# Optimization experiments

Hardware: AMD Instinct MI355X
Metric: run time of the kernel (lower is better)

Reference implementation:

```python
import jax, jax.numpy as jnp
import numpy as np

N, E, DIM, HID, LAYERS = 100000, 600000, 128, 256, 2
LN_EPS = 1e-5


def setup_inputs() -> dict:
    key = jax.random.key(0)
    ks = jax.random.split(key, 16)
    h = jax.random.normal(ks[0], (N, DIM), dtype=jnp.float32)
    edge_index = jax.random.randint(ks[1], (E, 2), 0, N, dtype=jnp.int64)
    edge_attr = jax.random.uniform(ks[2], (E, 1), dtype=jnp.float32)
    s = 0.02
    # edge MLP: Linear(2*DIM+1, HID) -> GELU -> Linear(HID, 1) -> Sigmoid
    edge_w1 = jax.random.normal(ks[3], (LAYERS, 2 * DIM + 1, HID), dtype=jnp.float32) * s
    edge_b1 = jnp.zeros((LAYERS, HID), dtype=jnp.float32)
    edge_w2 = jax.random.normal(ks[4], (LAYERS, HID, 1), dtype=jnp.float32) * s
    edge_b2 = jnp.zeros((LAYERS, 1), dtype=jnp.float32)
    # node MLP: Linear(2*DIM, HID) -> GELU -> Linear(HID, DIM)
    node_w1 = jax.random.normal(ks[5], (LAYERS, 2 * DIM, HID), dtype=jnp.float32) * s
    node_b1 = jnp.zeros((LAYERS, HID), dtype=jnp.float32)
    node_w2 = jax.random.normal(ks[6], (LAYERS, HID, DIM), dtype=jnp.float32) * s
    node_b2 = jnp.zeros((LAYERS, DIM), dtype=jnp.float32)
    ln_g = jnp.ones((LAYERS, DIM), dtype=jnp.float32)
    ln_b = jnp.zeros((LAYERS, DIM), dtype=jnp.float32)
    return {"h": h, "edge_index": edge_index, "edge_attr": edge_attr,
            "edge_w1": edge_w1, "edge_b1": edge_b1, "edge_w2": edge_w2, "edge_b2": edge_b2,
            "node_w1": node_w1, "node_b1": node_b1, "node_w2": node_w2, "node_b2": node_b2,
            "ln_g": ln_g, "ln_b": ln_b}


def _layernorm(x, g, b):
    mu = jnp.mean(x, axis=-1, keepdims=True)
    var = jnp.mean(jnp.square(x - mu), axis=-1, keepdims=True)
    return (x - mu) * jax.lax.rsqrt(var + LN_EPS) * g + b


def reference(h, edge_index, edge_attr, edge_w1, edge_b1, edge_w2, edge_b2,
              node_w1, node_b1, node_w2, node_b2, ln_g, ln_b):
    src = edge_index[:, 0]
    dst = edge_index[:, 1]
    n = h.shape[0]
    for i in range(LAYERS):
        h_src = h[src]                                  # [E, DIM]
        h_dst = h[dst]                                  # [E, DIM]
        x = jnp.concatenate([h_src, h_dst, edge_attr], axis=-1)  # [E, 2*DIM+1]
        g1 = jax.nn.gelu(x @ edge_w1[i] + edge_b1[i], approximate=False)
        gate = jax.nn.sigmoid(g1 @ edge_w2[i] + edge_b2[i])       # [E, 1]
        msg = h_src * gate                              # [E, DIM]
        agg = jax.ops.segment_sum(msg, dst, num_segments=n)       # [N, DIM]
        den = jax.ops.segment_sum(gate, dst, num_segments=n)      # [N, 1]
        agg = agg / jnp.maximum(den, 1e-6)
        u = jnp.concatenate([h, agg], axis=-1)          # [N, 2*DIM]
        upd = jax.nn.gelu(u @ node_w1[i] + node_b1[i], approximate=False) @ node_w2[i] + node_b2[i]
        h = _layernorm(h + upd, ln_g[i], ln_b[i])
    return h
```

## Files before the change

### kernel.cpp

```cpp
#include <hip/hip_runtime.h>
#include <math.h>

#define NNODE 100000
#define NEDGE 600000
#define DIM 128
#define HID 256
#define NLAYERS 2
#define PROJ_BLOCKS 1563

typedef short bf16x8 __attribute__((ext_vector_type(8)));
typedef short bf16x4 __attribute__((ext_vector_type(4)));
typedef float f32x4 __attribute__((ext_vector_type(4)));
typedef float f32x2 __attribute__((ext_vector_type(2)));

#define WK 136
#define WLD 264
#define LUTN 2048

__device__ __forceinline__ short f2bf(float x) {
    union { float f; unsigned u; } v; v.f = x;
    unsigned r = v.u + 0x7FFFu + ((v.u >> 16) & 1u);
    return (short)(r >> 16);
}
__device__ __forceinline__ float bf2f(short s) {
    union { unsigned u; float f; } v; v.u = ((unsigned)(unsigned short)s) << 16;
    return v.f;
}
__device__ __forceinline__ float gelu_fast(float x) {
    float e = exp2f(-2.4554673f * x);
    return x * __builtin_amdgcn_rcpf(1.0f + e);
}
__device__ __forceinline__ float lut_look(const float* __restrict__ lut, float x) {
    float t = fmaf(x, 128.f, 1024.5f);
    t = fminf(fmaxf(t, 0.f), 2047.f);
    return lut[(int)t];
}

__global__ void prep_weights(const float* __restrict__ ew1,
                             const float* __restrict__ eb1,
                             const float* __restrict__ ew2,
                             const float* __restrict__ nw1,
                             const float* __restrict__ nw2,
                             const float* __restrict__ h0,
                             const int* __restrict__ ei,
                             short* __restrict__ pW,
                             short* __restrict__ nW1T,
                             short* __restrict__ nW2T,
                             float* __restrict__ w1a_p,
                             float* __restrict__ b1_p,
                             float* __restrict__ w2_p,
                             short* __restrict__ hb,
                             unsigned char* __restrict__ h8,
                             float* __restrict__ luts,
                             int* __restrict__ deg)
{
    int idx = blockIdx.x * 256 + threadIdx.x;
    const int SZ1 = NLAYERS * 512 * 128;
    const int SZ2 = NLAYERS * 256 * 256;
    const int SZ3 = NLAYERS * 128 * 256;
    const int SZ4 = NLAYERS * 256;
    const int SZH = NNODE * DIM / 8;
    if (idx < SZ1) {
        int L = idx / (512 * 128); int rr = idx - L * 512 * 128;
        int r = rr >> 7, k = rr & 127;
        int srow = (r < 256) ? k : 128 + k;
        int scol = (r < 256) ? r : r - 256;
        pW[(size_t)L * 512 * WK + r * WK + k] = f2bf(ew1[(size_t)L * 257 * 256 + srow * 256 + scol]);
        return;
    }
    idx -= SZ1;
    if (idx < SZ2) {
        int L = idx >> 16, r = idx & 65535, n = r >> 8, k = r & 255;
        nW1T[(size_t)L * 256 * WLD + n * WLD + k] = f2bf(nw1[(size_t)L * 256 * 256 + k * 256 + n]);
        return;
    }
    idx -= SZ2;
    if (idx < SZ3) {
        int L = idx >> 15, r = idx & 32767, n = r >> 8, k = r & 255;
        nW2T[(size_t)L * 128 * WLD + n * WLD + k] = f2bf(nw2[(size_t)L * 256 * 128 + k * 128 + n]);
        return;
    }
    idx -= SZ3;
    if (idx < SZ4) {
        int L = idx >> 8, c = idx & 255;
        int cs = (c & ~63) | ((c & 3) * 16 + ((c >> 2) & 15));
        w1a_p[idx] = ew1[(size_t)L * 257 * 256 + 256 * 256 + cs];
        b1_p[idx]  = eb1[(size_t)L * 256 + cs];
        w2_p[idx]  = ew2[(size_t)L * 256 + cs];
        return;
    }
    idx -= SZ4;
    if (idx < SZH) {
        const float4* p = (const float4*)(h0 + (size_t)idx * 8);
        float4 a = p[0], b = p[1];
        bf16x8 t;
        t[0] = f2bf(a.x); t[1] = f2bf(a.y); t[2] = f2bf(a.z); t[3] = f2bf(a.w);
        t[4] = f2bf(b.x); t[5] = f2bf(b.y); t[6] = f2bf(b.z); t[7] = f2bf(b.w);
        *(bf16x8*)(hb + (size_t)idx * 8) = t;
        int wa = __builtin_amdgcn_cvt_pk_fp8_f32(a.x, a.y, 0, false);
        wa = __builtin_amdgcn_cvt_pk_fp8_f32(a.z, a.w, wa, true);
        int wb = __builtin_amdgcn_cvt_pk_fp8_f32(b.x, b.y, 0, false);
        wb = __builtin_amdgcn_cvt_pk_fp8_f32(b.z, b.w, wb, true);
        *(unsigned*)(h8 + (size_t)idx * 8) = (unsigned)wa;
        *(unsigned*)(h8 + (size_t)idx * 8 + 4) = (unsigned)wb;
        return;
    }
    idx -= SZH;
    if (idx < 2 * LUTN) {
        int i = idx & (LUTN - 1);
        float x = (float)(i - 1024) * (1.0f / 128.0f);
        float v;
        if (idx < LUTN) {
            v = 0.5f * x * (1.0f + erff(x * 0.70710678118654752f));
        } else {
            v = 1.0f / (1.0f + expf(-x));
        }
        luts[idx] = v;
        return;
    }
    idx -= 2 * LUTN;
    if (idx < NEDGE) {
        atomicAdd(&deg[ei[2 * idx + 1]], 1);
    }
}

__global__ void csr_scatter(const int* __restrict__ ei, const float* __restrict__ attr,
                            int* __restrict__ cursor, int2* __restrict__ epk) {
    int e = blockIdx.x * 256 + threadIdx.x;
    if (e >= NEDGE) return;
    int s = ei[2 * e], d = ei[2 * e + 1];
    int pos = atomicAdd(&cursor[d], 1);
    int2 pk; pk.x = s; pk.y = __float_as_int(attr[e]);
    epk[pos] = pk;
    if (e == 0) { int2 z; z.x = 0; z.y = 0; epk[NEDGE] = z; }
}

__device__ void scan_block512(const int* __restrict__ deg, int* __restrict__ rowptr,
                              int* __restrict__ cursor) {
    __shared__ int wsum[8];
    __shared__ int carry_s;
    const int tid = threadIdx.x, lane = tid & 63, wv = tid >> 6;
    if (tid == 0) carry_s = 0;
    __syncthreads();
    for (int base = 0; base < NNODE; base += 2048) {
        int i0 = base + tid * 4;
        int v0 = 0, v1 = 0, v2 = 0, v3 = 0;
        if (i0 + 3 < NNODE) {
            int4 q = *(const int4*)(deg + i0);
            v0 = q.x; v1 = q.y; v2 = q.z; v3 = q.w;
        } else if (i0 < NNODE) {
            v0 = deg[i0];
            if (i0 + 1 < NNODE) v1 = deg[i0 + 1];
            if (i0 + 2 < NNODE) v2 = deg[i0 + 2];
        }
        int tsum = v0 + v1 + v2 + v3;
        int x = tsum;
#pragma unroll
        for (int off = 1; off < 64; off <<= 1) {
            int y = __shfl_up(x, off);
            if (lane >= off) x += y;
        }
        if (lane == 63) wsum[wv] = x;
        __syncthreads();
        if (wv == 0) {
            int s = (lane < 8) ? wsum[lane] : 0;
#pragma unroll
            for (int off = 1; off < 8; off <<= 1) {
                int y = __shfl_up(s, off);
                if (lane >= off) s += y;
            }
            if (lane < 8) wsum[lane] = s;
        }
        __syncthreads();
        int carry = carry_s;
        int woff = wv ? wsum[wv - 1] : 0;
        int e0 = carry + woff + (x - tsum);
        if (i0 < NNODE)     { rowptr[i0] = e0;                cursor[i0] = e0; }
        if (i0 + 1 < NNODE) { int v = e0 + v0;                rowptr[i0+1] = v; cursor[i0+1] = v; }
        if (i0 + 2 < NNODE) { int v = e0 + v0 + v1;           rowptr[i0+2] = v; cursor[i0+2] = v; }
        if (i0 + 3 < NNODE) { int v = e0 + v0 + v1 + v2;      rowptr[i0+3] = v; cursor[i0+3] = v; }
        int total = wsum[7];
        __syncthreads();
        if (tid == 0) carry_s = carry + total;
        __syncthreads();
    }
    if (tid == 0) rowptr[NNODE] = carry_s;
}

__global__ __launch_bounds__(512, 2)
void proj_kernel(const short* __restrict__ hb,
                 const short* __restrict__ pW,
                 unsigned char* __restrict__ Ps8,
                 short* __restrict__ Pd,
                 const int* __restrict__ deg, int* __restrict__ rowptr,
                 int* __restrict__ cursor)
{
    if (blockIdx.x >= PROJ_BLOCKS) {
        scan_block512(deg, rowptr, cursor);
        return;
    }

    __shared__ short A[64][WK];
    const int tid = threadIdx.x;
    const int n0 = blockIdx.x * 64;

    for (int idx = tid; idx < 64 * 16; idx += 512) {
        int nl = idx >> 4, q = idx & 15;
        int gn = min(n0 + nl, NNODE - 1);
        *(bf16x8*)&A[nl][q * 8] = *(const bf16x8*)(hb + (size_t)gn * DIM + q * 8);
    }
    __syncthreads();

    const int lane = tid & 63;
    const int wv = tid >> 6;
    const int lrow = lane & 15;
    const int lkg = lane >> 4;

    f32x4 acc[4][4];
#pragma unroll
    for (int mi = 0; mi < 4; ++mi)
#pragma unroll
        for (int ni = 0; ni < 4; ++ni) acc[mi][ni] = (f32x4){0.f, 0.f, 0.f, 0.f};

    const short* xbase = &A[lrow][lkg * 8];
    const short* wbase = pW + (size_t)(wv * 64 + lrow) * WK + lkg * 8;

#pragma unroll
    for (int kt = 0; kt < 4; ++kt) {
        bf16x8 a[4], b[4];
#pragma unroll
        for (int mi = 0; mi < 4; ++mi)
            a[mi] = *(const bf16x8*)(xbase + mi * 16 * WK + kt * 32);
#pragma unroll
        for (int ni = 0; ni < 4; ++ni)
            b[ni] = *(const bf16x8*)(wbase + ni * 16 * WK + kt * 32);
#pragma unroll
        for (int mi = 0; mi < 4; ++mi)
#pragma unroll
            for (int ni = 0; ni < 4; ++ni)
                acc[mi][ni] = __builtin_amdgcn_mfma_f32_16x16x32_bf16(a[mi], b[ni], acc[mi][ni], 0, 0, 0);
    }

    const int cb = (wv & 3) * 64;
    if (wv < 4) {
#pragma unroll
        for (int mi = 0; mi < 4; ++mi)
#pragma unroll
            for (int reg = 0; reg < 4; ++reg) {
                int node = n0 + mi * 16 + lkg * 4 + reg;
                int w = __builtin_amdgcn_cvt_pk_fp8_f32(acc[mi][0][reg], acc[mi][1][reg], 0, false);
                w = __builtin_amdgcn_cvt_pk_fp8_f32(acc[mi][2][reg], acc[mi][3][reg], w, true);
                if (node < NNODE)
                    *(unsigned*)(Ps8 + (size_t)node * 256 + cb + lrow * 4) = (unsigned)w;
            }
    } else {
#pragma unroll
        for (int mi = 0; mi < 4; ++mi)
#pragma unroll
            for (int reg = 0; reg < 4; ++reg) {
                int node = n0 + mi * 16 + lkg * 4 + reg;
                bf16x4 t;
                t[0] = f2bf(acc[mi][0][reg]);
                t[1] = f2bf(acc[mi][1][reg]);
                t[2] = f2bf(acc[mi][2][reg]);
                t[3] = f2bf(acc[mi][3][reg]);
                if (node < NNODE)
                    *(bf16x4*)(Pd + (size_t)node * 256 + cb + lrow * 4) = t;
            }
    }
}

__global__ __launch_bounds__(256)
void edge_agg(const unsigned char* __restrict__ Ps8, const short* __restrict__ Pd,
              const unsigned char* __restrict__ h8,
              const int2* __restrict__ epk, const int* __restrict__ rowptr,
              const float* __restrict__ w1a_p, const float* __restrict__ b1_p,
              const float* __restrict__ w2_p, const float* __restrict__ b2,
              const float* __restrict__ luts,
              short* __restrict__ u2)
{
    __shared__ float sg[LUTN];
    __shared__ float ss[LUTN];

    const int tid = threadIdx.x;
#pragma unroll
    for (int i = 0; i < LUTN / 256; ++i) {
        sg[tid + i * 256] = luts[tid + i * 256];
        ss[tid + i * 256] = luts[LUTN + tid + i * 256];
    }
    __syncthreads();

    const int node = (blockIdx.x * 256 + tid) >> 6;
    const int lane = tid & 63;

    const int beg = __builtin_amdgcn_readfirstlane(rowptr[node]);
    const int end = __builtin_amdgcn_readfirstlane(rowptr[node + 1]);
    const int d = end - beg;

    const float4 w1av = ((const float4*)w1a_p)[lane];
    const float4 b1v  = ((const float4*)b1_p)[lane];
    const float4 w2v  = ((const float4*)w2_p)[lane];
    const float b2s = b2[0];

    bf16x4 pd = *(const bf16x4*)(Pd + (size_t)node * 256 + lane * 4);
    const float pb0 = bf2f(pd[0]) + b1v.x;
    const float pb1 = bf2f(pd[1]) + b1v.y;
    const float pb2 = bf2f(pd[2]) + b1v.z;
    const float pb3 = bf2f(pd[3]) + b1v.w;

    const unsigned pso = (unsigned)(lane * 4);
    const unsigned hvo = (unsigned)(lane * 2);

    float ax = 0.f, ay = 0.f, den = 0.f;

    if (d > 0) {
        const int dm = min(d, 64);
        const int dm1 = dm - 1;

        int2 sa0 = epk[beg + min(lane, d - 1)];
        int sl = sa0.x;
        float al = __int_as_float(sa0.y);

        auto gather = [&](int T, unsigned& PS, unsigned& HV) {
            int s_ = __shfl(sl, min(T, dm1));
            PS = *(const unsigned*)(Ps8 + (((unsigned)s_ << 8) + pso));
            HV = (unsigned)*(const unsigned short*)(h8 + (((unsigned)s_ << 7) + hvo));
        };
        auto edge_one = [&](float a, unsigned PSU, unsigned HVU) {
            f32x2 plo = __builtin_amdgcn_cvt_pk_f32_fp8((int)PSU, false);
            f32x2 phi = __builtin_amdgcn_cvt_pk_f32_fp8((int)PSU, true);
            float x0 = plo[0] + pb0 + a * w1av.x;
            float x1 = plo[1] + pb1 + a * w1av.y;
            float x2 = phi[0] + pb2 + a * w1av.z;
            float x3 = phi[1] + pb3 + a * w1av.w;
            float p = lut_look(sg, x0) * w2v.x + lut_look(sg, x1) * w2v.y +
                      lut_look(sg, x2) * w2v.z + lut_look(sg, x3) * w2v.w;
            p += __shfl_xor(p, 1);
            p += __shfl_xor(p, 2);
            p += __shfl_xor(p, 4);
            p += __shfl_xor(p, 8);
            p += __shfl_xor(p, 16);
            p += __shfl_xor(p, 32);
            float g = lut_look(ss, p + b2s);
            f32x2 hxy = __builtin_amdgcn_cvt_pk_f32_fp8((int)HVU, false);
            ax = fmaf(g, hxy[0], ax);
            ay = fmaf(g, hxy[1], ay);
            den += g;
        };

        unsigned pA0, pA1, pA2, pA3, hA0, hA1, hA2, hA3;
        unsigned pB0, pB1, pB2, pB3, hB0, hB1, hB2, hB3;
        gather(0, pA0, hA0); gather(1, pA1, hA1);
        gather(2, pA2, hA2); gather(3, pA3, hA3);

        for (int t = 0; t < dm; t += 4) {
            gather(t + 4, pB0, hB0); gather(t + 5, pB1, hB1);
            gather(t + 6, pB2, hB2); gather(t + 7, pB3, hB3);

            edge_one(__shfl(al, t), pA0, hA0);
            if (t + 1 < dm) edge_one(__shfl(al, t + 1), pA1, hA1);
            if (t + 2 < dm) edge_one(__shfl(al, t + 2), pA2, hA2);
            if (t + 3 < dm) edge_one(__shfl(al, t + 3), pA3, hA3);

            pA0 = pB0; pA1 = pB1; pA2 = pB2; pA3 = pB3;
            hA0 = hB0; hA1 = hB1; hA2 = hB2; hA3 = hB3;
        }

        for (int t2 = 64; t2 < d; ++t2) {
            int2 sa = epk[beg + t2];
            int s_ = __builtin_amdgcn_readfirstlane(sa.x);
            float a = __int_as_float(__builtin_amdgcn_readfirstlane(sa.y));
            unsigned PS = *(const unsigned*)(Ps8 + (((unsigned)s_ << 8) + pso));
            unsigned HV = (unsigned)*(const unsigned short*)(h8 + (((unsigned)s_ << 7) + hvo));
            edge_one(a, PS, HV);
        }
    }

    float dd = fmaxf(den, 1e-6f);
    float dinv = __builtin_amdgcn_rcpf(dd);
    dinv = dinv * (2.0f - dd * dinv);
    unsigned pk = (((unsigned)(unsigned short)f2bf(ay * dinv)) << 16) |
                  (unsigned)(unsigned short)f2bf(ax * dinv);
    *(unsigned*)(u2 + (size_t)node * 256 + lane * 2) = pk;
}

__global__ __launch_bounds__(256, 4)
void node_mlp(const float* __restrict__ hin,
              const short* __restrict__ hb,
              const short* __restrict__ u2,
              const short* __restrict__ W1T,
              const float* __restrict__ b1,
              const short* __restrict__ W2T,
              const float* __restrict__ b2,
              const float* __restrict__ lng, const float* __restrict__ lnb,
              float* __restrict__ hout, short* __restrict__ hb_out,
              unsigned char* __restrict__ h8_out)
{
    __shared__ short U[64][WLD];

    const int tid = threadIdx.x;
    const int n0 = blockIdx.x * 64;
    const int lane = tid & 63;
    const int wv = tid >> 6;

    for (int idx = tid; idx < 64 * 32; idx += 256) {
        int nl = idx >> 5, q = idx & 31;
        int gn = min(n0 + nl, NNODE - 1);
        const short* src = (q < 16) ? (hb + (size_t)gn * DIM + q * 8)
                                    : (u2 + (size_t)gn * 256 + (q - 16) * 8);
        *(bf16x8*)&U[nl][q * 8] = *(const bf16x8*)src;
    }
    __syncthreads();

    const int lrow = lane & 15;
    const int lkg = lane >> 4;
    const int n0w = wv * 64;

    f32x4 acc1[4][4];
#pragma unroll
    for (int mi = 0; mi < 4; ++mi)
#pragma unroll
        for (int ni = 0; ni < 4; ++ni) acc1[mi][ni] = (f32x4){0.f, 0.f, 0.f, 0.f};
    {
        const short* xbase = &U[lrow][lkg * 8];
        const short* wbase = W1T + (size_t)(n0w + lrow) * WLD + lkg * 8;
#pragma unroll
        for (int kt = 0; kt < 8; ++kt) {
            bf16x8 a[4], b[4];
#pragma unroll
            for (int mi = 0; mi < 4; ++mi)
                a[mi] = *(const bf16x8*)(xbase + mi * 16 * WLD + kt * 32);
#pragma unroll
            for (int ni = 0; ni < 4; ++ni)
                b[ni] = *(const bf16x8*)(wbase + ni * 16 * WLD + kt * 32);
#pragma unroll
            for (int mi = 0; mi < 4; ++mi)
#pragma unroll
                for (int ni = 0; ni < 4; ++ni)
                    acc1[mi][ni] = __builtin_amdgcn_mfma_f32_16x16x32_bf16(a[mi], b[ni], acc1[mi][ni], 0, 0, 0);
        }
    }
    __syncthreads();

    {
        float b1v[4];
#pragma unroll
        for (int ni = 0; ni < 4; ++ni) b1v[ni] = b1[n0w + ni * 16 + lrow];
#pragma unroll
        for (int mi = 0; mi < 4; ++mi)
#pragma unroll
            for (int ni = 0; ni < 4; ++ni)
#pragma unroll
                for (int reg = 0; reg < 4; ++reg) {
                    int row = mi * 16 + lkg * 4 + reg;
                    int col = n0w + ni * 16 + lrow;
                    U[row][col] = f2bf(gelu_fast(acc1[mi][ni][reg] + b1v[ni]));
                }
    }
    __syncthreads();

    f32x4 acc2[4][2];
#pragma unroll
    for (int mi = 0; mi < 4; ++mi)
#pragma unroll
        for (int ni = 0; ni < 2; ++ni) acc2[mi][ni] = (f32x4){0.f, 0.f, 0.f, 0.f};
    {
        const short* xbase = &U[lrow][lkg * 8];
        const short* wbase = W2T + (size_t)(wv * 32 + lrow) * WLD + lkg * 8;
#pragma unroll
        for (int kt = 0; kt < 8; ++kt) {
            bf16x8 a[4], b[2];
#pragma unroll
            for (int mi = 0; mi < 4; ++mi)
                a[mi] = *(const bf16x8*)(xbase + mi * 16 * WLD + kt * 32);
#pragma unroll
            for (int ni = 0; ni < 2; ++ni)
                b[ni] = *(const bf16x8*)(wbase + ni * 16 * WLD + kt * 32);
#pragma unroll
            for (int mi = 0; mi < 4; ++mi)
#pragma unroll
                for (int ni = 0; ni < 2; ++ni)
                    acc2[mi][ni] = __builtin_amdgcn_mfma_f32_16x16x32_bf16(a[mi], b[ni], acc2[mi][ni], 0, 0, 0);
        }
    }
    __syncthreads();

    float* R = (float*)&U[0][0];
    {
        float b2v[2];
#pragma unroll
        for (int ni = 0; ni < 2; ++ni) b2v[ni] = b2[wv * 32 + ni * 16 + lrow];
#pragma unroll
        for (int mi = 0; mi < 4; ++mi)
#pragma unroll
            for (int ni = 0; ni < 2; ++ni)
#pragma unroll
                for (int reg = 0; reg < 4; ++reg) {
                    int row = mi * 16 + lkg * 4 + reg;
                    int col = wv * 32 + ni * 16 + lrow;
                    R[row * 132 + col] = acc2[mi][ni][reg] + b2v[ni];
                }
    }
    __syncthreads();

#pragma unroll
    for (int ii = 0; ii < 16; ++ii) {
        int nl = wv * 16 + ii;
        int gn = n0 + nl;
        int gnc = min(gn, NNODE - 1);
        float rx = R[nl * 132 + lane * 2 + 0];
        float ry = R[nl * 132 + lane * 2 + 1];
        const float2 hh = *(const float2*)(hin + (size_t)gnc * DIM + lane * 2);
        float vx = rx + hh.x, vy = ry + hh.y;
        float s = vx + vy;
#pragma unroll
        for (int off = 32; off > 0; off >>= 1) s += __shfl_xor(s, off);
        float mu = s * (1.0f / 128.0f);
        float dx = vx - mu, dy = vy - mu;
        float q = dx * dx + dy * dy;
#pragma unroll
        for (int off = 32; off > 0; off >>= 1) q += __shfl_xor(q, off);
        float inv = rsqrtf(q * (1.0f / 128.0f) + 1e-5f);
        if (gn < NNODE) {
            const float2 gg = *(const float2*)(lng + lane * 2);
            const float2 bb = *(const float2*)(lnb + lane * 2);
            float ox = dx * inv * gg.x + bb.x;
            float oy = dy * inv * gg.y + bb.y;
            *(float2*)(hout + (size_t)gn * DIM + lane * 2) = make_float2(ox, oy);
            unsigned pk = ((unsigned)(unsigned short)f2bf(oy) << 16) |
                          (unsigned)(unsigned short)f2bf(ox);
            *(unsigned*)(hb_out + (size_t)gn * DIM + lane * 2) = pk;
            int w8 = __builtin_amdgcn_cvt_pk_fp8_f32(ox, oy, 0, false);
            *(unsigned short*)(h8_out + (size_t)gn * DIM + lane * 2) = (unsigned short)(w8 & 0xFFFF);
        }
    }
}

extern "C" void kernel_launch(void* const* d_in, const int* in_sizes, int n_in,
                              void* d_out, int out_size, void* d_ws, size_t ws_size,
                              hipStream_t stream) {
    const float* h0   = (const float*)d_in[0];
    const int*   ei   = (const int*)d_in[1];
    const float* attr = (const float*)d_in[2];
    const float* ew1  = (const float*)d_in[3];
    const float* eb1  = (const float*)d_in[4];
    const float* ew2  = (const float*)d_in[5];
    const float* eb2  = (const float*)d_in[6];
    const float* nw1  = (const float*)d_in[7];
    const float* nb1  = (const float*)d_in[8];
    const float* nw2  = (const float*)d_in[9];
    const float* nb2  = (const float*)d_in[10];
    const float* lng  = (const float*)d_in[11];
    const float* lnb  = (const float*)d_in[12];

    float* hout = (float*)d_out;

    char* p = (char*)d_ws;
    int*   rowptr = (int*)p;               p += sizeof(int) * (NNODE + 4);
    int*   cursor = (int*)p;               p += sizeof(int) * (NNODE + 4);
    int*   deg    = (int*)p;               p += sizeof(int) * (NNODE + 4);
    int2*  epk    = (int2*)p;              p += sizeof(int2) * (NEDGE + 1);
    short* hb     = (short*)p;             p += sizeof(short) * (size_t)NNODE * DIM;
    unsigned char* h8 = (unsigned char*)p; p += (size_t)NNODE * DIM;
    unsigned char* Ps8 = (unsigned char*)p; p += (size_t)NNODE * 256;
    short* Pd     = (short*)p;             p += sizeof(short) * (size_t)NNODE * 256;
    short* u2     = Pd;
    short* pW     = (short*)p;             p += sizeof(short) * (size_t)NLAYERS * 512 * WK;
    short* nW1T   = (short*)p;             p += sizeof(short) * (size_t)NLAYERS * 256 * WLD;
    short* nW2T   = (short*)p;             p += sizeof(short) * (size_t)NLAYERS * 128 * WLD;
    float* w1a_p  = (float*)p;             p += sizeof(float) * NLAYERS * 256;
    float* b1_p   = (float*)p;             p += sizeof(float) * NLAYERS * 256;
    float* w2_p   = (float*)p;             p += sizeof(float) * NLAYERS * 256;
    float* luts   = (float*)p;             p += sizeof(float) * 2 * LUTN;

    const int PREP_TOTAL = NLAYERS * 512 * 128 + NLAYERS * 256 * 256 +
                           NLAYERS * 128 * 256 + NLAYERS * 256 + NNODE * DIM / 8 +
                           2 * LUTN + NEDGE;

    hipMemsetAsync(deg, 0, (NNODE + 1) * sizeof(int), stream);
    prep_weights<<<(PREP_TOTAL + 255) / 256, 256, 0, stream>>>(
        ew1, eb1, ew2, nw1, nw2, h0, ei, pW, nW1T, nW2T, w1a_p, b1_p, w2_p, hb, h8, luts, deg);

    for (int L = 0; L < NLAYERS; ++L) {
        const float* hin = (L == 0) ? h0 : hout;
        proj_kernel<<<PROJ_BLOCKS + (L == 0 ? 1 : 0), 512, 0, stream>>>(
            hb, pW + (size_t)L * 512 * WK, Ps8, Pd, deg, rowptr, cursor);
        if (L == 0)
            csr_scatter<<<(NEDGE + 255) / 256, 256, 0, stream>>>(ei, attr, cursor, epk);
        edge_agg<<<NNODE / 4, 256, 0, stream>>>(
            Ps8, Pd, h8, epk, rowptr,
            w1a_p + (size_t)L * 256, b1_p + (size_t)L * 256,
            w2_p + (size_t)L * 256, eb2 + L, luts, u2);
        node_mlp<<<(NNODE + 63) / 64, 256, 0, stream>>>(
            hin, hb, u2,
            nW1T + (size_t)L * 256 * WLD, nb1 + (size_t)L * 256,
            nW2T + (size_t)L * 128 * WLD, nb2 + (size_t)L * 128,
            lng + (size_t)L * DIM, lnb + (size_t)L * DIM,
            hout, hb, h8);
    }
}
```

Measured before the change: 523.7 us.

## Process four edges per wavefront concurrently with 16-lane groups in edge aggregation

Restructures the per-node edge gather kernel so each 64-lane wavefront splits into four 16-lane groups, each handling a different edge at a time with 16 hidden units per lane. Loads become wider (uint4/uint2 per lane), the gate reduction needs only four shuffle steps, and the four groups' partial sums are combined with cross-group shuffles at the end. It also replaces the separate slow path for degree above 64 with a chunked loop over 64-edge blocks. The cost is more registers per lane (16-wide weight arrays and 8 accumulators), which may reduce occupancy, plus extra work on padded edges when the degree is not a multiple of four.

```diff
diff --git a/kernel.cpp b/kernel.cpp
--- a/kernel.cpp
+++ b/kernel.cpp
@@ -292,96 +292,127 @@
 
     const int node = (blockIdx.x * 256 + tid) >> 6;
     const int lane = tid & 63;
+    const int ll  = lane & 15;
+    const int grp = lane >> 4;
 
     const int beg = __builtin_amdgcn_readfirstlane(rowptr[node]);
     const int end = __builtin_amdgcn_readfirstlane(rowptr[node + 1]);
     const int d = end - beg;
 
-    const float4 w1av = ((const float4*)w1a_p)[lane];
-    const float4 b1v  = ((const float4*)b1_p)[lane];
-    const float4 w2v  = ((const float4*)w2_p)[lane];
     const float b2s = b2[0];
 
-    bf16x4 pd = *(const bf16x4*)(Pd + (size_t)node * 256 + lane * 4);
-    const float pb0 = bf2f(pd[0]) + b1v.x;
-    const float pb1 = bf2f(pd[1]) + b1v.y;
-    const float pb2 = bf2f(pd[2]) + b1v.z;
-    const float pb3 = bf2f(pd[3]) + b1v.w;
-
-    const unsigned pso = (unsigned)(lane * 4);
-    const unsigned hvo = (unsigned)(lane * 2);
-
-    float ax = 0.f, ay = 0.f, den = 0.f;
-
-    if (d > 0) {
-        const int dm = min(d, 64);
-        const int dm1 = dm - 1;
-
-        int2 sa0 = epk[beg + min(lane, d - 1)];
+    float w1a[16], w2c[16], pdb[16];
+#pragma unroll
+    for (int k = 0; k < 4; ++k) {
+        float4 ta = ((const float4*)w1a_p)[ll * 4 + k];
+        float4 tb = ((const float4*)b1_p)[ll * 4 + k];
+        float4 tc = ((const float4*)w2_p)[ll * 4 + k];
+        w1a[4 * k + 0] = ta.x; w1a[4 * k + 1] = ta.y; w1a[4 * k + 2] = ta.z; w1a[4 * k + 3] = ta.w;
+        pdb[4 * k + 0] = tb.x; pdb[4 * k + 1] = tb.y; pdb[4 * k + 2] = tb.z; pdb[4 * k + 3] = tb.w;
+        w2c[4 * k + 0] = tc.x; w2c[4 * k + 1] = tc.y; w2c[4 * k + 2] = tc.z; w2c[4 * k + 3] = tc.w;
+    }
+    {
+        bf16x8 pd0 = *(const bf16x8*)(Pd + (size_t)node * 256 + ll * 16);
+        bf16x8 pd1 = *(const bf16x8*)(Pd + (size_t)node * 256 + ll * 16 + 8);
+#pragma unroll
+        for (int j = 0; j < 8; ++j) pdb[j] += bf2f(pd0[j]);
+#pragma unroll
+        for (int j = 0; j < 8; ++j) pdb[8 + j] += bf2f(pd1[j]);
+    }
+
+    float ax[8];
+#pragma unroll
+    for (int j = 0; j < 8; ++j) ax[j] = 0.f;
+    float den = 0.f;
+
+    const unsigned pso = (unsigned)(ll * 16);
+    const unsigned hvo = (unsigned)(ll * 8);
+
+    for (int base = 0; base < d; base += 64) {
+        const int cn = min(64, d - base);
+        const int cl = cn - 1;
+        int2 sa0 = epk[beg + base + min(lane, cl)];
         int sl = sa0.x;
         float al = __int_as_float(sa0.y);
-
-        auto gather = [&](int T, unsigned& PS, unsigned& HV) {
-            int s_ = __shfl(sl, min(T, dm1));
-            PS = *(const unsigned*)(Ps8 + (((unsigned)s_ << 8) + pso));
-            HV = (unsigned)*(const unsigned short*)(h8 + (((unsigned)s_ << 7) + hvo));
-        };
-        auto edge_one = [&](float a, unsigned PSU, unsigned HVU) {
-            f32x2 plo = __builtin_amdgcn_cvt_pk_f32_fp8((int)PSU, false);
-            f32x2 phi = __builtin_amdgcn_cvt_pk_f32_fp8((int)PSU, true);
-            float x0 = plo[0] + pb0 + a * w1av.x;
-            float x1 = plo[1] + pb1 + a * w1av.y;
-            float x2 = phi[0] + pb2 + a * w1av.z;
-            float x3 = phi[1] + pb3 + a * w1av.w;
-            float p = lut_look(sg, x0) * w2v.x + lut_look(sg, x1) * w2v.y +
-                      lut_look(sg, x2) * w2v.z + lut_look(sg, x3) * w2v.w;
+        const int iters = (cn + 3) >> 2;
+
+        int eA = grp;
+        int srcA = __shfl(sl, min(eA, cl));
+        float aA = __shfl(al, min(eA, cl));
+        uint4 psA = *(const uint4*)(Ps8 + (((size_t)(unsigned)srcA) << 8) + pso);
+        uint2 hA  = *(const uint2*)(h8 + (((size_t)(unsigned)srcA) << 7) + hvo);
+
+        for (int t = 0; t < iters; ++t) {
+            int eB = ((t + 1) << 2) + grp;
+            int srcB = __shfl(sl, min(eB, cl));
+            float aB = __shfl(al, min(eB, cl));
+            uint4 psB = *(const uint4*)(Ps8 + (((size_t)(unsigned)srcB) << 8) + pso);
+            uint2 hB  = *(const uint2*)(h8 + (((size_t)(unsigned)srcB) << 7) + hvo);
+
+            float p = 0.f;
+            {
+                unsigned dw[4] = {psA.x, psA.y, psA.z, psA.w};
+#pragma unroll
+                for (int k = 0; k < 4; ++k) {
+                    f32x2 lo = __builtin_amdgcn_cvt_pk_f32_fp8((int)dw[k], false);
+                    f32x2 hi = __builtin_amdgcn_cvt_pk_f32_fp8((int)dw[k], true);
+                    float x0 = lo[0] + pdb[4 * k + 0] + aA * w1a[4 * k + 0];
+                    float x1 = lo[1] + pdb[4 * k + 1] + aA * w1a[4 * k + 1];
+                    float x2 = hi[0] + pdb[4 * k + 2] + aA * w1a[4 * k + 2];
+                    float x3 = hi[1] + pdb[4 * k + 3] + aA * w1a[4 * k + 3];
+                    p += lut_look(sg, x0) * w2c[4 * k + 0];
+                    p += lut_look(sg, x1) * w2c[4 * k + 1];
+                    p += lut_look(sg, x2) * w2c[4 * k + 2];
+                    p += lut_look(sg, x3) * w2c[4 * k + 3];
+                }
+            }
             p += __shfl_xor(p, 1);
             p += __shfl_xor(p, 2);
             p += __shfl_xor(p, 4);
             p += __shfl_xor(p, 8);
-            p += __shfl_xor(p, 16);
-            p += __shfl_xor(p, 32);
             float g = lut_look(ss, p + b2s);
-            f32x2 hxy = __builtin_amdgcn_cvt_pk_f32_fp8((int)HVU, false);
-            ax = fmaf(g, hxy[0], ax);
-            ay = fmaf(g, hxy[1], ay);
-            den += g;
-        };
-
-        unsigned pA0, pA1, pA2, pA3, hA0, hA1, hA2, hA3;
-        unsigned pB0, pB1, pB2, pB3, hB0, hB1, hB2, hB3;
-        gather(0, pA0, hA0); gather(1, pA1, hA1);
-        gather(2, pA2, hA2); gather(3, pA3, hA3);
-
-        for (int t = 0; t < dm; t += 4) {
-            gather(t + 4, pB0, hB0); gather(t + 5, pB1, hB1);
-            gather(t + 6, pB2, hB2); gather(t + 7, pB3, hB3);
-
-            edge_one(__shfl(al, t), pA0, hA0);
-            if (t + 1 < dm) edge_one(__shfl(al, t + 1), pA1, hA1);
-            if (t + 2 < dm) edge_one(__shfl(al, t + 2), pA2, hA2);
-            if (t + 3 < dm) edge_one(__shfl(al, t + 3), pA3, hA3);
-
-            pA0 = pB0; pA1 = pB1; pA2 = pB2; pA3 = pB3;
-            hA0 = hB0; hA1 = hB1; hA2 = hB2; hA3 = hB3;
-        }
-
-        for (int t2 = 64; t2 < d; ++t2) {
-            int2 sa = epk[beg + t2];
-            int s_ = __builtin_amdgcn_readfirstlane(sa.x);
-            float a = __int_as_float(__builtin_amdgcn_readfirstlane(sa.y));
-            unsigned PS = *(const unsigned*)(Ps8 + (((unsigned)s_ << 8) + pso));
-            unsigned HV = (unsigned)*(const unsigned short*)(h8 + (((unsigned)s_ << 7) + hvo));
-            edge_one(a, PS, HV);
-        }
-    }
+            if (((t << 2) + grp) >= cn) g = 0.f;
+
+            {
+                f32x2 h01 = __builtin_amdgcn_cvt_pk_f32_fp8((int)hA.x, false);
+                f32x2 h23 = __builtin_amdgcn_cvt_pk_f32_fp8((int)hA.x, true);
+                f32x2 h45 = __builtin_amdgcn_cvt_pk_f32_fp8((int)hA.y, false);
+                f32x2 h67 = __builtin_amdgcn_cvt_pk_f32_fp8((int)hA.y, true);
+                ax[0] = fmaf(g, h01[0], ax[0]);
+                ax[1] = fmaf(g, h01[1], ax[1]);
+                ax[2] = fmaf(g, h23[0], ax[2]);
+                ax[3] = fmaf(g, h23[1], ax[3]);
+                ax[4] = fmaf(g, h45[0], ax[4]);
+                ax[5] = fmaf(g, h45[1], ax[5]);
+                ax[6] = fmaf(g, h67[0], ax[6]);
+                ax[7] = fmaf(g, h67[1], ax[7]);
+                den += g;
+            }
+
+            psA = psB; hA = hB; aA = aB;
+        }
+    }
+
+#pragma unroll
+    for (int j = 0; j < 8; ++j) {
+        ax[j] += __shfl_xor(ax[j], 16);
+        ax[j] += __shfl_xor(ax[j], 32);
+    }
+    den += __shfl_xor(den, 16);
+    den += __shfl_xor(den, 32);
 
     float dd = fmaxf(den, 1e-6f);
     float dinv = __builtin_amdgcn_rcpf(dd);
     dinv = dinv * (2.0f - dd * dinv);
-    unsigned pk = (((unsigned)(unsigned short)f2bf(ay * dinv)) << 16) |
-                  (unsigned)(unsigned short)f2bf(ax * dinv);
-    *(unsigned*)(u2 + (size_t)node * 256 + lane * 2) = pk;
+
+    if (grp == 0) {
+        uint4 o;
+        o.x = (((unsigned)(unsigned short)f2bf(ax[1] * dinv)) << 16) | (unsigned)(unsigned short)f2bf(ax[0] * dinv);
+        o.y = (((unsigned)(unsigned short)f2bf(ax[3] * dinv)) << 16) | (unsigned)(unsigned short)f2bf(ax[2] * dinv);
+        o.z = (((unsigned)(unsigned short)f2bf(ax[5] * dinv)) << 16) | (unsigned)(unsigned short)f2bf(ax[4] * dinv);
+        o.w = (((unsigned)(unsigned short)f2bf(ax[7] * dinv)) << 16) | (unsigned)(unsigned short)f2bf(ax[6] * dinv);
+        *(uint4*)(u2 + (size_t)node * 256 + ll * 8) = o;
+    }
 }
 
 __global__ __launch_bounds__(256, 4)
```

Measured after the change: 635.9 us. 21.4% more time.
